# Optimization experiments

Hardware: AMD Instinct MI355X
Metric: run time of the kernel (lower is better)

Reference implementation:

```python
import jax, jax.numpy as jnp
import numpy as np

# Fixed Gauss-Legendre quadrature on [-A, A] replacing scipy.integrate.quadrature
A = 5.0
NQ = 64
_x, _w = np.polynomial.legendre.leggauss(NQ)
GL_X = jnp.asarray(_x * A, dtype=jnp.float32)  # nodes scaled to [-5, 5]
# Fold exp(-z^2/2)/sqrt(2*pi) and interval scaling into the weights
GL_W_EFF = jnp.asarray(_w * A * np.exp(-(_x * A) ** 2 / 2.0) / np.sqrt(2.0 * np.pi), dtype=jnp.float32)

# given_params=True constants
SIG_M1, SIG_M2, SIG_I = 1.0, 1.0, 1.0
SIG_M1N1, SIG_M2N2 = 1.0, 0.5
SIG_N1I, SIG_N2I = 0.5, 1.9
SIG_M1W, SIG_M2W = 2.8, -2.2
TAU, DT = 100.0, 20.0


def setup_inputs() -> dict:
    key = jax.random.key(0)
    B, T = 8192, 2048
    u = jax.random.normal(key, (B, T), dtype=jnp.float32)
    return {"u": u}


def reference(u):
    B, T = u.shape
    alpha = jnp.float32(DT / TAU)

    def step(carry, u_t):
        k1, k2, v = carry  # each [B]
        delta = jnp.sqrt(SIG_M1**2 * k1**2 + SIG_M2**2 * k2**2 + SIG_I**2 * u_t**2)  # [B]
        # gauss_int[b] = int_{-A}^{A} (1 - tanh(delta_b z)^2) exp(-z^2/2) dz / sqrt(2pi)
        dphi = 1.0 - jnp.tanh(delta[:, None] * GL_X[None, :]) ** 2  # [B, NQ]
        gauss_int = dphi @ GL_W_EFF  # [B]
        k1_new = k1 + (-k1 + SIG_M1N1 * gauss_int * k1 + SIG_N1I * gauss_int * v) * alpha
        k2_new = k2 + (-k2 + SIG_M2N2 * gauss_int * k2 + SIG_N2I * gauss_int * v) * alpha
        v_new = v + (-v + u_t) * alpha
        z = SIG_M1W * k1_new + SIG_M2W * k2_new
        return (k1_new, k2_new, v_new), z

    zeros = jnp.zeros((B,), dtype=u.dtype)
    _, z_seq = jax.lax.scan(step, (zeros, zeros, zeros), u.T)  # z_seq: [T, B]
    # z_hist: [B, T+1], column 0 is the zero initial state
    z_hist = jnp.concatenate([zeros[:, None], z_seq.T], axis=1)
    return z_hist
```

## Files before the change

kernel.cpp:

```cpp
#include <hip/hip_runtime.h>
#include <math.h>


#define Bsz   8192
#define Tlen  2048
#define TP1   2049
#define NQ    64
#define NG    2049
#define NTAB2 2048
#define INV_H 32.0f
#define CHUNKS 16
#define CLEN  128
#define WARM  128
#define BLOCK 256
#define SIM_GRID (32 * CHUNKS)
#define SROW  33

#define WS_TAB 128

__device__ __forceinline__ void bar_nodrain() {
    asm volatile("s_waitcnt lgkmcnt(0)" ::: "memory");
    __builtin_amdgcn_s_barrier();
}
__device__ __forceinline__ void ds_fence() {
    asm volatile("s_waitcnt lgkmcnt(0)" ::: "memory");
}

__global__ __launch_bounds__(256) void setup_kernel(float* __restrict__ ws,
                                                    float* __restrict__ out) {
    __shared__ float  fx[NQ], fw[NQ];
    __shared__ double inv[NQ + 1];
    const int tid = threadIdx.x;
    if (tid <= NQ) inv[tid] = (tid == 0) ? 0.0 : 1.0 / (double)tid;
    __syncthreads();
    if (tid < NQ) {
        double z = cos(3.14159265358979323846 * (tid + 0.75) / (NQ + 0.5));
        double p1 = 1.0, p2 = 0.0, pp = 1.0;
        for (int it = 0; it < 4; ++it) {
            p1 = 1.0; p2 = 0.0;
            for (int j = 1; j <= NQ; ++j) {
                double p3 = p2; p2 = p1;
                p1 = ((2.0 * j - 1.0) * z * p2 - (j - 1.0) * p3) * inv[j];
            }
            pp = NQ * (z * p1 - p2) / (z * z - 1.0);
            if (it < 3) z -= p1 / pp;
        }
        double w  = 2.0 / ((1.0 - z * z) * pp * pp);
        double xs = z * 5.0;
        fx[tid] = (float)xs;
        fw[tid] = (float)(w * 5.0 * exp(-0.5 * xs * xs) * 0.3989422804014327);
    }
    __syncthreads();
    const int j = blockIdx.x * 256 + tid;
    if (j < NG) {
        const float d = sqrtf((float)j * (1.0f / INV_H));
        float acc = 0.0f;
        #pragma unroll 8
        for (int q = 0; q < NQ; ++q) {
            float t = tanhf(d * fx[q]);
            acc = fmaf(fw[q], 1.0f - t * t, acc);
        }
        ws[WS_TAB + j] = acc;
    }
    out[(size_t)j * TP1] = 0.0f;
}

__device__ __forceinline__ float step_one(float uu, float& k1, float& k2,
                                          float& v, const float2* s_tab) {
    float s   = fmaf(k1, k1, fmaf(k2, k2, uu * uu));
    float idx = fminf(s * INV_H, 2046.999f);
    int   i0  = (int)idx;
    float f   = idx - (float)i0;
    float2 g2 = s_tab[i0];
    float g   = fmaf(f, g2.y - g2.x, g2.x);
    float gv  = g * v;
    float nk1 = fmaf(k1, fmaf(0.2f, g, 0.8f), 0.10f * gv);
    float nk2 = fmaf(k2, fmaf(0.1f, g, 0.8f), 0.38f * gv);
    v  = fmaf(0.2f, uu - v, v);
    k1 = nk1; k2 = nk2;
    return fmaf(2.8f, nk1, -2.2f * nk2);
}

#define GLOAD(G, t) { _Pragma("unroll")                                       \
    for (int r = 0; r < 8; ++r)                                               \
        G[r] = *(const float4*)(up + (size_t)r * 8 * Tlen + (t)); }

#define STAGE(G) { asm volatile("" ::: "memory");  _Pragma("unroll")          \
    for (int r = 0; r < 8; ++r) {                                             \
        int b8 = (8 * r + srow) * SROW + scol;                                \
        sb[b8] = G[r].x; sb[b8+1] = G[r].y; sb[b8+2] = G[r].z;                \
        sb[b8+3] = G[r].w; }                                                  \
    ds_fence(); }

#define READBACK() { asm volatile("" ::: "memory"); _Pragma("unroll")         \
    for (int j = 0; j < 32; ++j) U[j] = sb[lbase + j];                        \
    ds_fence(); }

#define FLUSH(h) { const int cb = t_out + 1 + 64 * (h);                       \
    _Pragma("unroll") for (int p = 0; p < 2; ++p) {                           \
        asm volatile("" ::: "memory");                                        \
        _Pragma("unroll") for (int j = 0; j < 32; ++j)                        \
            sb[lbase + j] = zz[p * 32 + j];                                   \
        ds_fence();                                                           \
        _Pragma("unroll") for (int kk = 0; kk < 32; ++kk) {                   \
            int row = 2 * kk + rh;                                            \
            out[(size_t)(rowb + row) * TP1 + cb + p * 32 + col] =             \
                sb[row * SROW + col];                                         \
        }                                                                     \
        ds_fence(); } }

__global__ __launch_bounds__(BLOCK, 2) void sim_kernel(const float* __restrict__ u,
                                                       const float* __restrict__ ws,
                                                       float* __restrict__ out) {
    __shared__ float2 s_tab[NTAB2];
    __shared__ float  s_st[4][64 * SROW];
    const int tid = threadIdx.x;
    const int w   = tid >> 6;
    const int l   = tid & 63;
    float* sb = s_st[w];

    const int c    = blockIdx.x >> 5;
    const int bb   = blockIdx.x & 31;
    const int rowb = bb * 256 + w * 64;
    const int t_out   = c * CLEN;
    const int t_begin = (t_out >= WARM) ? (t_out - WARM) : 0;

    const int srow = l >> 3;
    const int scol = (l & 7) * 4;
    const float* __restrict__ up = u + (size_t)(rowb + srow) * Tlen + scol;
    const int lbase = l * SROW;

    float4 G[8];
    GLOAD(G, t_begin);

    {
        const float* g = ws + WS_TAB;
        #pragma unroll
        for (int i = 0; i < NTAB2 / (BLOCK * 4); ++i) {
            int k = (i * BLOCK + tid) * 4;
            float4 a = *(const float4*)(g + k);
            float  b = g[k + 4];
            s_tab[k + 0] = make_float2(a.x, a.y);
            s_tab[k + 1] = make_float2(a.y, a.z);
            s_tab[k + 2] = make_float2(a.z, a.w);
            s_tab[k + 3] = make_float2(a.w, b);
        }
    }
    bar_nodrain();

    STAGE(G);
    GLOAD(G, t_begin + 32);

    float k1 = 0.f, k2 = 0.f, v = 0.f;
    float U[32];

    for (int tb = t_begin; tb < t_out; tb += 32) {
        READBACK();
        STAGE(G);
        GLOAD(G, tb + 64);
        #pragma unroll
        for (int t2 = 0; t2 < 32; ++t2)
            step_one(U[t2], k1, k2, v, s_tab);
    }

    const int col = l & 31;
    const int rh  = l >> 5;
    float zz[64];
    #pragma unroll
    for (int k = 0; k < 4; ++k) {
        const int tb = t_out + 32 * k;
        READBACK();
        if (k == 2) FLUSH(0);
        STAGE(G);
        int tn = tb + 64;
        if (tn > Tlen - 32) tn = Tlen - 32;
        GLOAD(G, tn);
        #pragma unroll
        for (int t2 = 0; t2 < 32; ++t2)
            zz[(k & 1) * 32 + t2] = step_one(U[t2], k1, k2, v, s_tab);
    }
    FLUSH(1);
}

extern "C" void kernel_launch(void* const* d_in, const int* in_sizes, int n_in,
                              void* d_out, int out_size, void* d_ws, size_t ws_size,
                              hipStream_t stream) {
    const float* u = (const float*)d_in[0];
    float* out = (float*)d_out;
    float* ws  = (float*)d_ws;
    setup_kernel<<<32, 256, 0, stream>>>(ws, out);
    sim_kernel<<<SIM_GRID, BLOCK, 0, stream>>>(u, ws, out);
}
```

Baseline: 145.3 us.

## Replace LDS lookup table with Chebyshev fit of gauss integral in rsqrt variable

```diff
diff --git a/kernel.cpp b/kernel.cpp
--- a/kernel.cpp
+++ b/kernel.cpp
@@ -6,9 +6,7 @@
 #define Tlen  2048
 #define TP1   2049
 #define NQ    64
-#define NG    2049
-#define NTAB2 2048
-#define INV_H 32.0f
+#define NCH   16
 #define CHUNKS 16
 #define CLEN  128
 #define WARM  128
@@ -16,63 +14,95 @@
 #define SIM_GRID (32 * CHUNKS)
 #define SROW  33
 
-#define WS_TAB 128
-
-__device__ __forceinline__ void bar_nodrain() {
-    asm volatile("s_waitcnt lgkmcnt(0)" ::: "memory");
-    __builtin_amdgcn_s_barrier();
-}
+#define PI_D 3.14159265358979323846
+#define B_D  1.5707963267948966
+#define D_YM 0.5496216
+#define D_YR 0.4503784
+
 __device__ __forceinline__ void ds_fence() {
     asm volatile("s_waitcnt lgkmcnt(0)" ::: "memory");
 }
 
 __global__ __launch_bounds__(256) void setup_kernel(float* __restrict__ ws,
                                                     float* __restrict__ out) {
-    __shared__ float  fx[NQ], fw[NQ];
-    __shared__ double inv[NQ + 1];
     const int tid = threadIdx.x;
-    if (tid <= NQ) inv[tid] = (tid == 0) ? 0.0 : 1.0 / (double)tid;
-    __syncthreads();
-    if (tid < NQ) {
-        double z = cos(3.14159265358979323846 * (tid + 0.75) / (NQ + 0.5));
-        double p1 = 1.0, p2 = 0.0, pp = 1.0;
-        for (int it = 0; it < 4; ++it) {
-            p1 = 1.0; p2 = 0.0;
-            for (int j = 1; j <= NQ; ++j) {
-                double p3 = p2; p2 = p1;
-                p1 = ((2.0 * j - 1.0) * z * p2 - (j - 1.0) * p3) * inv[j];
+    if (blockIdx.x == 0) {
+        __shared__ double dxs[NQ], dwe[NQ], dh[NCH];
+        __shared__ double inv[NQ + 1];
+        if (tid <= NQ) inv[tid] = (tid == 0) ? 0.0 : 1.0 / (double)tid;
+        __syncthreads();
+        if (tid < NQ) {
+            double z = cos(PI_D * (tid + 0.75) / (NQ + 0.5));
+            double p1 = 1.0, p2 = 0.0, pp = 1.0;
+            for (int it = 0; it < 4; ++it) {
+                p1 = 1.0; p2 = 0.0;
+                for (int j = 1; j <= NQ; ++j) {
+                    double p3 = p2; p2 = p1;
+                    p1 = ((2.0 * j - 1.0) * z * p2 - (j - 1.0) * p3) * inv[j];
+                }
+                pp = NQ * (z * p1 - p2) / (z * z - 1.0);
+                if (it < 3) z -= p1 / pp;
             }
-            pp = NQ * (z * p1 - p2) / (z * z - 1.0);
-            if (it < 3) z -= p1 / pp;
+            double w  = 2.0 / ((1.0 - z * z) * pp * pp);
+            double xs = z * 5.0;
+            dxs[tid] = xs;
+            dwe[tid] = w * 5.0 * exp(-0.5 * xs * xs) * 0.3989422804014327;
         }
-        double w  = 2.0 / ((1.0 - z * z) * pp * pp);
-        double xs = z * 5.0;
-        fx[tid] = (float)xs;
-        fw[tid] = (float)(w * 5.0 * exp(-0.5 * xs * xs) * 0.3989422804014327);
+        __syncthreads();
+        if (tid < NCH) {
+            double th = PI_D * (tid + 0.5) / NCH;
+            double yk = D_YM + D_YR * cos(th);
+            double sk = (1.0 / (yk * yk) - 1.0) / B_D;
+            double dk = sqrt(sk);
+            double acc = 0.0;
+            for (int q = 0; q < NQ; ++q) {
+                double t0 = tanh(dk * dxs[q]);
+                acc += dwe[q] * (1.0 - t0 * t0);
+            }
+            dh[tid] = acc / yk;
+        }
+        __syncthreads();
+        if (tid < NCH) {
+            double cj = 0.0;
+            for (int k = 0; k < NCH; ++k)
+                cj += dh[k] * cos((double)tid * PI_D * (k + 0.5) / NCH);
+            cj *= 2.0 / NCH;
+            if (tid == 0) cj *= 0.5;
+            ws[tid] = (float)cj;
+        }
     }
-    __syncthreads();
     const int j = blockIdx.x * 256 + tid;
-    if (j < NG) {
-        const float d = sqrtf((float)j * (1.0f / INV_H));
-        float acc = 0.0f;
-        #pragma unroll 8
-        for (int q = 0; q < NQ; ++q) {
-            float t = tanhf(d * fx[q]);
-            acc = fmaf(fw[q], 1.0f - t * t, acc);
-        }
-        ws[WS_TAB + j] = acc;
-    }
     out[(size_t)j * TP1] = 0.0f;
 }
 
 __device__ __forceinline__ float step_one(float uu, float& k1, float& k2,
-                                          float& v, const float2* s_tab) {
-    float s   = fmaf(k1, k1, fmaf(k2, k2, uu * uu));
-    float idx = fminf(s * INV_H, 2046.999f);
-    int   i0  = (int)idx;
-    float f   = idx - (float)i0;
-    float2 g2 = s_tab[i0];
-    float g   = fmaf(f, g2.y - g2.x, g2.x);
+                                          float& v, float4 cA, float4 cB,
+                                          float4 cC, float4 cD) {
+    float s  = fmaf(k1, k1, fmaf(k2, k2, uu * uu));
+    s        = fminf(s, 63.9f);
+    float ys = fmaf((float)B_D, s, 1.0f);
+    float y;
+    asm("v_rsq_f32 %0, %1" : "=v"(y) : "v"(ys));
+    float t  = fmaf(y, (float)(1.0 / D_YR), -(float)(D_YM / D_YR));
+    float u2 = fmaf(t + t, t, -1.0f);
+    float tu = u2 + u2;
+    float b7 = cD.z;
+    float b6 = fmaf(tu, b7, cD.x);
+    float b5 = fmaf(tu, b6, cC.z - b7);
+    float b4 = fmaf(tu, b5, cC.x - b6);
+    float b3 = fmaf(tu, b4, cB.z - b5);
+    float b2 = fmaf(tu, b3, cB.x - b4);
+    float b1 = fmaf(tu, b2, cA.z - b3);
+    float SE = fmaf(u2, b1, cA.x - b2);
+    float a7 = cD.w;
+    float a6 = fmaf(tu, a7, cD.y);
+    float a5 = fmaf(tu, a6, cC.w - a7);
+    float a4 = fmaf(tu, a5, cC.y - a6);
+    float a3 = fmaf(tu, a4, cB.w - a5);
+    float a2 = fmaf(tu, a3, cB.y - a4);
+    float a1 = fmaf(tu, a2, cA.w - a3);
+    float a0 = fmaf(tu, a1, cA.y - a2);
+    float g  = fmaf(t, a0 - a1, SE) * y;
     float gv  = g * v;
     float nk1 = fmaf(k1, fmaf(0.2f, g, 0.8f), 0.10f * gv);
     float nk2 = fmaf(k2, fmaf(0.1f, g, 0.8f), 0.38f * gv);
@@ -112,8 +142,7 @@
 __global__ __launch_bounds__(BLOCK, 2) void sim_kernel(const float* __restrict__ u,
                                                        const float* __restrict__ ws,
                                                        float* __restrict__ out) {
-    __shared__ float2 s_tab[NTAB2];
-    __shared__ float  s_st[4][64 * SROW];
+    __shared__ float s_st[4][64 * SROW];
     const int tid = threadIdx.x;
     const int w   = tid >> 6;
     const int l   = tid & 63;
@@ -133,20 +162,8 @@
     float4 G[8];
     GLOAD(G, t_begin);
 
-    {
-        const float* g = ws + WS_TAB;
-        #pragma unroll
-        for (int i = 0; i < NTAB2 / (BLOCK * 4); ++i) {
-            int k = (i * BLOCK + tid) * 4;
-            float4 a = *(const float4*)(g + k);
-            float  b = g[k + 4];
-            s_tab[k + 0] = make_float2(a.x, a.y);
-            s_tab[k + 1] = make_float2(a.y, a.z);
-            s_tab[k + 2] = make_float2(a.z, a.w);
-            s_tab[k + 3] = make_float2(a.w, b);
-        }
-    }
-    bar_nodrain();
+    const float4* ws4 = (const float4*)ws;
+    float4 cA = ws4[0], cB = ws4[1], cC = ws4[2], cD = ws4[3];
 
     STAGE(G);
     GLOAD(G, t_begin + 32);
@@ -160,7 +177,7 @@
         GLOAD(G, tb + 64);
         #pragma unroll
         for (int t2 = 0; t2 < 32; ++t2)
-            step_one(U[t2], k1, k2, v, s_tab);
+            step_one(U[t2], k1, k2, v, cA, cB, cC, cD);
     }
 
     const int col = l & 31;
@@ -177,7 +194,7 @@
         GLOAD(G, tn);
         #pragma unroll
         for (int t2 = 0; t2 < 32; ++t2)
-            zz[(k & 1) * 32 + t2] = step_one(U[t2], k1, k2, v, s_tab);
+            zz[(k & 1) * 32 + t2] = step_one(U[t2], k1, k2, v, cA, cB, cC, cD);
     }
     FLUSH(1);
 }
```

New measurement: 175.0 us. 1.2x slower.

## Halve rows per wave and shrink LDS to raise occupancy of recurrence

Applied to the files above, without the earlier changes.

```diff
diff --git a/kernel.cpp b/kernel.cpp
--- a/kernel.cpp
+++ b/kernel.cpp
@@ -7,14 +7,14 @@
 #define TP1   2049
 #define NQ    64
 #define NG    2049
-#define NTAB2 2048
 #define INV_H 32.0f
 #define CHUNKS 16
 #define CLEN  128
 #define WARM  128
 #define BLOCK 256
-#define SIM_GRID (32 * CHUNKS)
+#define RPW   32
 #define SROW  33
+#define SIM_GRID (64 * CHUNKS)
 
 #define WS_TAB 128
 
@@ -66,13 +66,14 @@
 }
 
 __device__ __forceinline__ float step_one(float uu, float& k1, float& k2,
-                                          float& v, const float2* s_tab) {
+                                          float& v, const float* tab) {
     float s   = fmaf(k1, k1, fmaf(k2, k2, uu * uu));
     float idx = fminf(s * INV_H, 2046.999f);
     int   i0  = (int)idx;
     float f   = idx - (float)i0;
-    float2 g2 = s_tab[i0];
-    float g   = fmaf(f, g2.y - g2.x, g2.x);
+    float ga  = tab[i0];
+    float gb  = tab[i0 + 1];
+    float g   = fmaf(f, gb - ga, ga);
     float gv  = g * v;
     float nk1 = fmaf(k1, fmaf(0.2f, g, 0.8f), 0.10f * gv);
     float nk2 = fmaf(k2, fmaf(0.1f, g, 0.8f), 0.38f * gv);
@@ -82,69 +83,60 @@
 }
 
 #define GLOAD(G, t) { _Pragma("unroll")                                       \
-    for (int r = 0; r < 8; ++r)                                               \
+    for (int r = 0; r < 4; ++r)                                               \
         G[r] = *(const float4*)(up + (size_t)r * 8 * Tlen + (t)); }
 
 #define STAGE(G) { asm volatile("" ::: "memory");  _Pragma("unroll")          \
-    for (int r = 0; r < 8; ++r) {                                             \
+    for (int r = 0; r < 4; ++r) {                                             \
         int b8 = (8 * r + srow) * SROW + scol;                                \
         sb[b8] = G[r].x; sb[b8+1] = G[r].y; sb[b8+2] = G[r].z;                \
         sb[b8+3] = G[r].w; }                                                  \
     ds_fence(); }
 
-#define READBACK() { asm volatile("" ::: "memory"); _Pragma("unroll")         \
-    for (int j = 0; j < 32; ++j) U[j] = sb[lbase + j];                        \
-    ds_fence(); }
-
 #define FLUSH(h) { const int cb = t_out + 1 + 64 * (h);                       \
     _Pragma("unroll") for (int p = 0; p < 2; ++p) {                           \
         asm volatile("" ::: "memory");                                        \
-        _Pragma("unroll") for (int j = 0; j < 32; ++j)                        \
-            sb[lbase + j] = zz[p * 32 + j];                                   \
+        if (l < 32) { _Pragma("unroll") for (int j = 0; j < 32; ++j)          \
+            sb[lbase + j] = zz[p * 32 + j]; }                                 \
         ds_fence();                                                           \
-        _Pragma("unroll") for (int kk = 0; kk < 32; ++kk) {                   \
-            int row = 2 * kk + rh;                                            \
-            out[(size_t)(rowb + row) * TP1 + cb + p * 32 + col] =             \
-                sb[row * SROW + col];                                         \
+        _Pragma("unroll") for (int kk = 0; kk < 16; ++kk) {                   \
+            int row = 2 * kk + (l >> 5);                                      \
+            out[(size_t)(rowb + row) * TP1 + cb + p * 32 + (l & 31)] =        \
+                sb[row * SROW + (l & 31)];                                    \
         }                                                                     \
         ds_fence(); } }
 
-__global__ __launch_bounds__(BLOCK, 2) void sim_kernel(const float* __restrict__ u,
+__global__ __launch_bounds__(BLOCK, 4) void sim_kernel(const float* __restrict__ u,
                                                        const float* __restrict__ ws,
                                                        float* __restrict__ out) {
-    __shared__ float2 s_tab[NTAB2];
-    __shared__ float  s_st[4][64 * SROW];
+    __shared__ float s_tabS[NG];
+    __shared__ float s_st[4][RPW * SROW];
     const int tid = threadIdx.x;
     const int w   = tid >> 6;
     const int l   = tid & 63;
     float* sb = s_st[w];
 
-    const int c    = blockIdx.x >> 5;
-    const int bb   = blockIdx.x & 31;
-    const int rowb = bb * 256 + w * 64;
+    const int c    = blockIdx.x >> 6;
+    const int rb   = blockIdx.x & 63;
+    const int rowb = rb * 128 + w * RPW;
     const int t_out   = c * CLEN;
     const int t_begin = (t_out >= WARM) ? (t_out - WARM) : 0;
 
     const int srow = l >> 3;
     const int scol = (l & 7) * 4;
     const float* __restrict__ up = u + (size_t)(rowb + srow) * Tlen + scol;
-    const int lbase = l * SROW;
+    const int lbase = (l & 31) * SROW;
 
-    float4 G[8];
+    float4 G[4];
     GLOAD(G, t_begin);
 
     {
         const float* g = ws + WS_TAB;
-        #pragma unroll
-        for (int i = 0; i < NTAB2 / (BLOCK * 4); ++i) {
-            int k = (i * BLOCK + tid) * 4;
-            float4 a = *(const float4*)(g + k);
-            float  b = g[k + 4];
-            s_tab[k + 0] = make_float2(a.x, a.y);
-            s_tab[k + 1] = make_float2(a.y, a.z);
-            s_tab[k + 2] = make_float2(a.z, a.w);
-            s_tab[k + 3] = make_float2(a.w, b);
-        }
+        float4 a0 = *(const float4*)(g + tid * 8);
+        float4 a1 = *(const float4*)(g + tid * 8 + 4);
+        *(float4*)&s_tabS[tid * 8]     = a0;
+        *(float4*)&s_tabS[tid * 8 + 4] = a1;
+        if (tid == 0) s_tabS[2048] = g[2048];
     }
     bar_nodrain();
 
@@ -152,32 +144,29 @@
     GLOAD(G, t_begin + 32);
 
     float k1 = 0.f, k2 = 0.f, v = 0.f;
-    float U[32];
 
     for (int tb = t_begin; tb < t_out; tb += 32) {
-        READBACK();
+        #pragma unroll
+        for (int t2 = 0; t2 < 32; ++t2)
+            step_one(sb[lbase + t2], k1, k2, v, s_tabS);
+        ds_fence();
         STAGE(G);
         GLOAD(G, tb + 64);
+    }
+
+    float zz[64];
+    #pragma unroll
+    for (int k2w = 0; k2w < 4; ++k2w) {
         #pragma unroll
         for (int t2 = 0; t2 < 32; ++t2)
-            step_one(U[t2], k1, k2, v, s_tab);
-    }
-
-    const int col = l & 31;
-    const int rh  = l >> 5;
-    float zz[64];
-    #pragma unroll
-    for (int k = 0; k < 4; ++k) {
-        const int tb = t_out + 32 * k;
-        READBACK();
-        if (k == 2) FLUSH(0);
+            zz[(k2w & 1) * 32 + t2] = step_one(sb[lbase + t2], k1, k2, v, s_tabS);
+        ds_fence();
+        if (k2w == 1) FLUSH(0);
+        if (k2w == 3) break;
         STAGE(G);
-        int tn = tb + 64;
+        int tn = t_out + 32 * k2w + 64;
         if (tn > Tlen - 32) tn = Tlen - 32;
         GLOAD(G, tn);
-        #pragma unroll
-        for (int t2 = 0; t2 < 32; ++t2)
-            zz[(k & 1) * 32 + t2] = step_one(U[t2], k1, k2, v, s_tab);
     }
     FLUSH(1);
 }
```

Result: slower. 191.2 us (+31.6%).
